# Kernel tuning notes

Measured on AMD Instinct MI355X. Metric: run time of the kernel, lower is better.

## Reference

```python
import jax, jax.numpy as jnp
import numpy as np

N, E, M = 8192, 32768, 2048
D, H1, C = 768, 8, 768
NEG_SLOPE = 0.2


def gat_conv(x, src, dst, W, att_src, att_dst, bias, heads, out_ch):
    # PyG GATConv (eval mode, concat=True, add_self_loops already applied to src/dst)
    n = x.shape[0]
    h = (x @ W).reshape(n, heads, out_ch)                      # [N,H,C]
    a_src = jnp.einsum('nhc,hc->nh', h, att_src)               # [N,H]
    a_dst = jnp.einsum('nhc,hc->nh', h, att_dst)
    e = jax.nn.leaky_relu(a_src[src] + a_dst[dst], NEG_SLOPE)  # [E',H]
    # softmax over incoming edges of each dst node
    m = jax.ops.segment_max(e, dst, num_segments=n)
    e = jnp.exp(e - m[dst])
    denom = jax.ops.segment_sum(e, dst, num_segments=n)
    alpha = e / (denom[dst] + 1e-16)                           # [E',H]
    msg = h[src] * alpha[:, :, None]                           # [E',H,C]
    out = jax.ops.segment_sum(msg, dst, num_segments=n)        # [N,H,C]
    return out.reshape(n, heads * out_ch) + bias


def setup_inputs() -> dict:
    key = jax.random.key(0)
    ks = jax.random.split(key, 16)
    s = 0.02
    inp = {
        'x': jax.random.normal(ks[0], (N, D), jnp.float32),
        'edge_index': jax.random.randint(ks[1], (2, E), 0, N, jnp.int64),
        'mask_idx': jax.random.randint(ks[2], (M,), 0, N, jnp.int64),
        'W1': jax.random.normal(ks[3], (D, H1 * C), jnp.float32) * s,
        'att_src1': jax.random.normal(ks[4], (H1, C), jnp.float32) * s,
        'att_dst1': jax.random.normal(ks[5], (H1, C), jnp.float32) * s,
        'b1': jnp.zeros((H1 * C,), jnp.float32),
        'W2': jax.random.normal(ks[6], (H1 * C, C), jnp.float32) * s,
        'att_src2': jax.random.normal(ks[7], (1, C), jnp.float32) * s,
        'att_dst2': jax.random.normal(ks[8], (1, C), jnp.float32) * s,
        'b2': jnp.zeros((C,), jnp.float32),
        # fc: 1536 -> 768, classifier: 768 -> 2
        'fc_w': jax.random.normal(ks[9], (2 * C, C), jnp.float32) * s,
        'fc_b': jnp.zeros((C,), jnp.float32),
        'cls_w': jax.random.normal(ks[10], (C, 2), jnp.float32) * s,
        'cls_b': jnp.zeros((2,), jnp.float32),
    }
    return inp


def reference(x, edge_index, mask_idx, W1, att_src1, att_dst1, b1,
              W2, att_src2, att_dst2, b2, fc_w, fc_b, cls_w, cls_b):
    n = x.shape[0]
    loops = jnp.arange(n, dtype=edge_index.dtype)
    src = jnp.concatenate([edge_index[0], loops])   # PyG default add_self_loops
    dst = jnp.concatenate([edge_index[1], loops])
    h = gat_conv(x, src, dst, W1, att_src1, att_dst1, b1, H1, C)   # [N, 6144]
    h = jax.nn.elu(h)
    h = gat_conv(h, src, dst, W2, att_src2, att_dst2, b2, 1, C)    # [N, 768]
    x_gemb = h[mask_idx]                                           # [M, 768]
    x_emb = x[mask_idx]                                            # [M, 768]
    out = jnp.concatenate([x_gemb, x_emb], axis=1) @ fc_w + fc_b   # [M, 768]
    out = out @ cls_w + cls_b                                      # [M, 2]
    return out
```

## Files before the change

kernel.cpp:

```cpp
#include <hip/hip_runtime.h>

typedef unsigned short ushort_t;
typedef __attribute__((ext_vector_type(8))) __bf16 bf16x8;
typedef __attribute__((ext_vector_type(8))) unsigned short ushort8;
typedef __attribute__((ext_vector_type(4))) unsigned short ushort4v;
typedef __attribute__((ext_vector_type(4))) float f32x4;

#define N_NODES 8192
#define NODE_MASK 8191
#define E_EDGES 32768
#define E_TOT   40960
#define M_MASK  2048
#define D_IN    768
#define C_CH    768
#define F1      6144

typedef __attribute__((address_space(1))) const void* gas_ptr;
typedef __attribute__((address_space(3))) void* las_ptr;

__device__ __forceinline__ float bf2f(ushort_t u) {
    union { unsigned int i; float f; } v; v.i = ((unsigned int)u) << 16; return v.f;
}
__device__ __forceinline__ ushort_t f2bf(float f) {
    union { float f; unsigned int i; } v; v.f = f;
    unsigned int r = v.i + 0x7fffu + ((v.i >> 16) & 1u);
    return (ushort_t)(r >> 16);
}

__global__ void init_kernel(int* deg, int* fill, int* flags) {
    int i = blockIdx.x * 256 + threadIdx.x;
    if (i < N_NODES) { deg[i] = 0; fill[i] = 0; }
    if (i < 2) flags[i] = 0;
}
__global__ void detect_kernel(const int* __restrict__ raw, int nhalf, int* __restrict__ flag) {
    int i = blockIdx.x * 256 + threadIdx.x;
    if (i < nhalf && raw[2 * i + 1] != 0) atomicOr(flag, 1);
}
__global__ void convert_idx_kernel(const void* __restrict__ raw, int n,
                                   const int* __restrict__ flag, int* __restrict__ out) {
    int i = blockIdx.x * 256 + threadIdx.x;
    if (i >= n) return;
    int v = (*flag) ? ((const int*)raw)[i] : (int)((const long long*)raw)[i];
    out[i] = v & NODE_MASK;
}

__global__ void cvt_bf16_kernel(const float* __restrict__ in, ushort_t* __restrict__ out, int n4) {
    int i = blockIdx.x * 256 + threadIdx.x;
    if (i >= n4) return;
    f32x4 v = *(const f32x4*)(in + i * 4);
    ushort_t o0 = f2bf(v[0]), o1 = f2bf(v[1]), o2 = f2bf(v[2]), o3 = f2bf(v[3]);
    unsigned long long pk = (unsigned long long)o0 | ((unsigned long long)o1 << 16)
                          | ((unsigned long long)o2 << 32) | ((unsigned long long)o3 << 48);
    *(unsigned long long*)(out + i * 4) = pk;
}

__global__ __launch_bounds__(256) void transpose_cvt_kernel(
    const float* __restrict__ in, ushort_t* __restrict__ out, int R, int Ccols)
{
    __shared__ ushort_t tile[32][33];
    int tx = threadIdx.x & 31, ty = threadIdx.x >> 5;
    int x  = blockIdx.x * 32 + tx;
    int y0 = blockIdx.y * 32;
#pragma unroll
    for (int i = 0; i < 4; ++i)
        tile[ty + i * 8][tx] = f2bf(in[(size_t)(y0 + ty + i * 8) * Ccols + x]);
    __syncthreads();
#pragma unroll
    for (int i = 0; i < 4; ++i)
        out[(size_t)(blockIdx.x * 32 + ty + i * 8) * R + y0 + tx] = tile[tx][ty + i * 8];
}

__global__ __launch_bounds__(256) void gemm_bt_kernel(
    const ushort_t* __restrict__ A, const ushort_t* __restrict__ Bt,
    ushort_t* __restrict__ C, const float* __restrict__ bias,
    int M, int N, int K)
{
    __shared__ ushort_t lsA[128 * 64];
    __shared__ ushort_t lsB[128 * 64];

    const int tid  = threadIdx.x;
    const int lane = tid & 63;
    const int wave = tid >> 6;
    const int wm = wave >> 1, wn = wave & 1;
    const int bx = blockIdx.x, by = blockIdx.y;

    const f32x4 zero = {0.f, 0.f, 0.f, 0.f};
    f32x4 acc[4][4];
#pragma unroll
    for (int i = 0; i < 4; ++i)
#pragma unroll
        for (int j = 0; j < 4; ++j) acc[i][j] = zero;

    const int l8 = lane >> 3;
    const int c8 = lane & 7;
    const int q  = lane >> 4;
    const int rl = lane & 15;

    for (int kt = 0; kt < K; kt += 64) {
        __syncthreads();
#pragma unroll
        for (int i = 0; i < 4; ++i) {
            int rbase = wave * 32 + i * 8;
            int row   = rbase + l8;
            int gch   = c8 ^ (row & 7);
            const ushort_t* gA = A  + (size_t)(by * 128 + row) * K + kt + gch * 8;
            const ushort_t* gB = Bt + (size_t)(bx * 128 + row) * K + kt + gch * 8;
            __builtin_amdgcn_global_load_lds((gas_ptr)gA, (las_ptr)(lsA + rbase * 64), 16, 0, 0);
            __builtin_amdgcn_global_load_lds((gas_ptr)gB, (las_ptr)(lsB + rbase * 64), 16, 0, 0);
        }
        __syncthreads();
#pragma unroll
        for (int s = 0; s < 2; ++s) {
            bf16x8 af[4], bfv[4];
#pragma unroll
            for (int i = 0; i < 4; ++i) {
                int Ra = wm * 64 + i * 16 + rl;
                af[i]  = *(const bf16x8*)(lsA + Ra * 64 + (((s * 4 + q) ^ (Ra & 7)) * 8));
                int Rb = wn * 64 + i * 16 + rl;
                bfv[i] = *(const bf16x8*)(lsB + Rb * 64 + (((s * 4 + q) ^ (Rb & 7)) * 8));
            }
#pragma unroll
            for (int i = 0; i < 4; ++i)
#pragma unroll
                for (int j = 0; j < 4; ++j)
                    acc[i][j] = __builtin_amdgcn_mfma_f32_16x16x32_bf16(af[i], bfv[j], acc[i][j], 0, 0, 0);
        }
    }
#pragma unroll
    for (int j = 0; j < 4; ++j) {
        int col = bx * 128 + wn * 64 + j * 16 + rl;
        float bv = bias ? bias[col] : 0.0f;
#pragma unroll
        for (int i = 0; i < 4; ++i) {
#pragma unroll
            for (int t = 0; t < 4; ++t) {
                int row = by * 128 + wm * 64 + i * 16 + q * 4 + t;
                C[(size_t)row * N + col] = f2bf(acc[i][j][t] + bv);
            }
        }
    }
}

#define NBX2 6
#define NBY2 64
#define NSPLIT 2

__global__ __launch_bounds__(256) void gemm_bt_splitk_kernel(
    const ushort_t* __restrict__ A, const ushort_t* __restrict__ Bt,
    float* __restrict__ Cpart, int M, int N, int K)
{
    __shared__ ushort_t lsA[128 * 64];
    __shared__ ushort_t lsB[128 * 64];

    const int tid  = threadIdx.x;
    const int lane = tid & 63;
    const int wave = tid >> 6;
    const int wm = wave >> 1, wn = wave & 1;

    const int d    = blockIdx.x;
    const int xcd  = d & 7;
    const int slot = d >> 3;
    const int bx   = slot % NBX2;
    const int grp  = xcd * 16 + slot / NBX2;
    const int by   = grp & (NBY2 - 1);
    const int bz   = grp >> 6;

    const int kh  = K >> 1;
    const int kt0 = bz * kh;
    float* __restrict__ Cp = Cpart + (size_t)bz * M * N;

    const f32x4 zero = {0.f, 0.f, 0.f, 0.f};
    f32x4 acc[4][4];
#pragma unroll
    for (int i = 0; i < 4; ++i)
#pragma unroll
        for (int j = 0; j < 4; ++j) acc[i][j] = zero;

    const int l8 = lane >> 3;
    const int c8 = lane & 7;
    const int q  = lane >> 4;
    const int rl = lane & 15;

    for (int kt = kt0; kt < kt0 + kh; kt += 64) {
        __syncthreads();
#pragma unroll
        for (int i = 0; i < 4; ++i) {
            int rbase = wave * 32 + i * 8;
            int row   = rbase + l8;
            int gch   = c8 ^ (row & 7);
            const ushort_t* gA = A  + (size_t)(by * 128 + row) * K + kt + gch * 8;
            const ushort_t* gB = Bt + (size_t)(bx * 128 + row) * K + kt + gch * 8;
            __builtin_amdgcn_global_load_lds((gas_ptr)gA, (las_ptr)(lsA + rbase * 64), 16, 0, 0);
            __builtin_amdgcn_global_load_lds((gas_ptr)gB, (las_ptr)(lsB + rbase * 64), 16, 0, 0);
        }
        __syncthreads();
#pragma unroll
        for (int s = 0; s < 2; ++s) {
            bf16x8 af[4], bfv[4];
#pragma unroll
            for (int i = 0; i < 4; ++i) {
                int Ra = wm * 64 + i * 16 + rl;
                af[i]  = *(const bf16x8*)(lsA + Ra * 64 + (((s * 4 + q) ^ (Ra & 7)) * 8));
                int Rb = wn * 64 + i * 16 + rl;
                bfv[i] = *(const bf16x8*)(lsB + Rb * 64 + (((s * 4 + q) ^ (Rb & 7)) * 8));
            }
#pragma unroll
            for (int i = 0; i < 4; ++i)
#pragma unroll
                for (int j = 0; j < 4; ++j)
                    acc[i][j] = __builtin_amdgcn_mfma_f32_16x16x32_bf16(af[i], bfv[j], acc[i][j], 0, 0, 0);
        }
    }
#pragma unroll
    for (int j = 0; j < 4; ++j) {
        int col = bx * 128 + wn * 64 + j * 16 + rl;
#pragma unroll
        for (int i = 0; i < 4; ++i) {
#pragma unroll
            for (int t = 0; t < 4; ++t) {
                int row = by * 128 + wm * 64 + i * 16 + q * 4 + t;
                Cp[(size_t)row * N + col] = acc[i][j][t];
            }
        }
    }
}

__global__ __launch_bounds__(192) void splitk_reduce_att_kernel(
    const float* __restrict__ P0, const float* __restrict__ P1,
    ushort_t* __restrict__ out, const float* __restrict__ as2,
    const float* __restrict__ ad2, float* __restrict__ a_s, float* __restrict__ a_d)
{
    const int n = blockIdx.x, tid = threadIdx.x;
    const int c0 = tid * 4;
    f32x4 a = *(const f32x4*)(P0 + (size_t)n * C_CH + c0);
    f32x4 b = *(const f32x4*)(P1 + (size_t)n * C_CH + c0);
    f32x4 ws = *(const f32x4*)(as2 + c0);
    f32x4 wd = *(const f32x4*)(ad2 + c0);
    float s1 = 0.f, s2 = 0.f;
    ushort_t o[4];
#pragma unroll
    for (int k = 0; k < 4; ++k) {
        float v = a[k] + b[k];
        o[k] = f2bf(v);
        s1 += v * ws[k];
        s2 += v * wd[k];
    }
    unsigned long long pk = (unsigned long long)o[0] | ((unsigned long long)o[1] << 16)
                          | ((unsigned long long)o[2] << 32) | ((unsigned long long)o[3] << 48);
    *(unsigned long long*)(out + (size_t)n * C_CH + c0) = pk;

    __shared__ float red[2][3];
#pragma unroll
    for (int off = 32; off > 0; off >>= 1) {
        s1 += __shfl_down(s1, off);
        s2 += __shfl_down(s2, off);
    }
    const int lane = tid & 63, wv = tid >> 6;
    if (lane == 0) { red[0][wv] = s1; red[1][wv] = s2; }
    __syncthreads();
    if (tid == 0) {
        a_s[n] = red[0][0] + red[0][1] + red[0][2];
        a_d[n] = red[1][0] + red[1][1] + red[1][2];
    }
}

__global__ void indeg_kernel(const int* __restrict__ eic, int* __restrict__ deg) {
    int e = blockIdx.x * 256 + threadIdx.x;
    if (e >= E_TOT) return;
    int dst = (e < E_EDGES) ? eic[E_EDGES + e] : (e - E_EDGES);
    atomicAdd(&deg[dst], 1);
}
__global__ __launch_bounds__(256) void scan_kernel(const int* __restrict__ deg, int* __restrict__ rowptr) {
    __shared__ int part[256];
    int t = threadIdx.x;
    int local[32];
    int s = 0;
#pragma unroll
    for (int i = 0; i < 32; ++i) { local[i] = deg[t * 32 + i]; s += local[i]; }
    part[t] = s;
    __syncthreads();
    for (int off = 1; off < 256; off <<= 1) {
        int v = (t >= off) ? part[t - off] : 0;
        __syncthreads();
        part[t] += v;
        __syncthreads();
    }
    int run = (t == 0) ? 0 : part[t - 1];
#pragma unroll
    for (int i = 0; i < 32; ++i) { rowptr[t * 32 + i] = run; run += local[i]; }
    if (t == 255) rowptr[N_NODES] = run;
}
__global__ void scatter_kernel(const int* __restrict__ eic, const int* __restrict__ rowptr,
                               int* __restrict__ fill, int* __restrict__ csr_src) {
    int e = blockIdx.x * 256 + threadIdx.x;
    if (e >= E_TOT) return;
    int src, dst;
    if (e < E_EDGES) { src = eic[e]; dst = eic[E_EDGES + e]; }
    else             { src = e - E_EDGES; dst = src; }
    int pos = rowptr[dst] + atomicAdd(&fill[dst], 1);
    csr_src[pos] = src;
}

__global__ __launch_bounds__(256) void att_kernel(
    const ushort_t* __restrict__ h, const float* __restrict__ att_s,
    const float* __restrict__ att_d, float* __restrict__ a_s, float* __restrict__ a_d,
    int heads, int stride)
{
    int gid  = blockIdx.x * 4 + (threadIdx.x >> 6);
    int lane = threadIdx.x & 63;
    int n = gid / heads, hd = gid % heads;
    const ushort_t* hp = h + (size_t)n * stride + hd * C_CH;
    const float* sp = att_s + hd * C_CH;
    const float* dp = att_d + hd * C_CH;
    float s1 = 0.f, s2 = 0.f;
#pragma unroll
    for (int j = 0; j < 3; ++j) {
        int o = j * 256 + lane * 4;
        ushort4v hv = *(const ushort4v*)(hp + o);
        f32x4 sv = *(const f32x4*)(sp + o);
        f32x4 dv = *(const f32x4*)(dp + o);
#pragma unroll
        for (int k = 0; k < 4; ++k) {
            float f = bf2f(hv[k]);
            s1 += f * sv[k];
            s2 += f * dv[k];
        }
    }
#pragma unroll
    for (int off = 32; off > 0; off >>= 1) {
        s1 += __shfl_down(s1, off);
        s2 += __shfl_down(s2, off);
    }
    if (lane == 0) { a_s[gid] = s1; a_d[gid] = s2; }
}

__global__ __launch_bounds__(192) void agg8_kernel(
    const ushort_t* __restrict__ h, const float* __restrict__ a_s, const float* __restrict__ a_d,
    const int* __restrict__ rowptr, const int* __restrict__ csr_src,
    const float* __restrict__ bias, ushort_t* __restrict__ out)
{
    const int n = blockIdx.x;
    const int half = blockIdx.y;
    const int tid = threadIdx.x;
    const int base = rowptr[n];
    const int deg  = rowptr[n + 1] - base;

    __shared__ float s_m[8], s_rd[8], s_adst[8];
    __shared__ int   s_src[64];
    __shared__ float s_w[64][8];

    if (tid < 8) {
        float adst = a_d[n * 8 + tid];
        float m = -1e30f;
        for (int e = 0; e < deg; ++e) {
            float scv = a_s[csr_src[base + e] * 8 + tid] + adst;
            scv = scv > 0.f ? scv : 0.2f * scv;
            m = fmaxf(m, scv);
        }
        float den = 0.f;
        for (int e = 0; e < deg; ++e) {
            float scv = a_s[csr_src[base + e] * 8 + tid] + adst;
            scv = scv > 0.f ? scv : 0.2f * scv;
            den += __expf(scv - m);
        }
        s_m[tid] = m; s_rd[tid] = 1.0f / (den + 1e-16f); s_adst[tid] = adst;
    }
    __syncthreads();

    float acc[16];
#pragma unroll
    for (int i = 0; i < 16; ++i) acc[i] = 0.f;
    const int c0   = half * 3072 + tid * 16;
    const int myhd = (half << 2) + tid / 48;

    for (int cs = 0; cs < deg; cs += 64) {
        int cnt = min(64, deg - cs);
        __syncthreads();
        for (int idx = tid; idx < cnt; idx += 192) s_src[idx] = csr_src[base + cs + idx];
        __syncthreads();
        for (int idx = tid; idx < cnt * 8; idx += 192) {
            int e = idx >> 3, hd = idx & 7;
            float scv = a_s[s_src[e] * 8 + hd] + s_adst[hd];
            scv = scv > 0.f ? scv : 0.2f * scv;
            s_w[e][hd] = __expf(scv - s_m[hd]) * s_rd[hd];
        }
        __syncthreads();
        int e = 0;
        for (; e + 1 < cnt; e += 2) {
            const ushort_t* hp0 = h + (size_t)s_src[e] * F1 + c0;
            const ushort_t* hp1 = h + (size_t)s_src[e + 1] * F1 + c0;
            ushort8 a0 = *(const ushort8*)(hp0);
            ushort8 a1 = *(const ushort8*)(hp0 + 8);
            ushort8 b0 = *(const ushort8*)(hp1);
            ushort8 b1 = *(const ushort8*)(hp1 + 8);
            float w0 = s_w[e][myhd], w1 = s_w[e + 1][myhd];
#pragma unroll
            for (int i = 0; i < 8; ++i) {
                acc[i]     += w0 * bf2f(a0[i]) + w1 * bf2f(b0[i]);
                acc[8 + i] += w0 * bf2f(a1[i]) + w1 * bf2f(b1[i]);
            }
        }
        if (e < cnt) {
            const ushort_t* hp0 = h + (size_t)s_src[e] * F1 + c0;
            ushort8 a0 = *(const ushort8*)(hp0);
            ushort8 a1 = *(const ushort8*)(hp0 + 8);
            float w0 = s_w[e][myhd];
#pragma unroll
            for (int i = 0; i < 8; ++i) {
                acc[i]     += w0 * bf2f(a0[i]);
                acc[8 + i] += w0 * bf2f(a1[i]);
            }
        }
    }
#pragma unroll
    for (int i = 0; i < 16; ++i) {
        float v = acc[i] + bias[c0 + i];
        v = v > 0.f ? v : (__expf(v) - 1.0f);
        out[(size_t)n * F1 + c0 + i] = f2bf(v);
    }
}

__global__ __launch_bounds__(256) void agg1_kernel(
    const ushort_t* __restrict__ h, const float* __restrict__ a_s, const float* __restrict__ a_d,
    const int* __restrict__ rowptr, const int* __restrict__ csr_src,
    const float* __restrict__ bias, ushort_t* __restrict__ out)
{
    const int n = blockIdx.x;
    const int tid = threadIdx.x;
    const int base = rowptr[n];
    const int deg  = rowptr[n + 1] - base;
    __shared__ float s_m, s_rd, s_adst;
    __shared__ int   s_src[64];
    __shared__ float s_w[64];
    if (tid == 0) {
        float adst = a_d[n];
        float m = -1e30f;
        for (int e = 0; e < deg; ++e) {
            float scv = a_s[csr_src[base + e]] + adst;
            scv = scv > 0.f ? scv : 0.2f * scv;
            m = fmaxf(m, scv);
        }
        float den = 0.f;
        for (int e = 0; e < deg; ++e) {
            float scv = a_s[csr_src[base + e]] + adst;
            scv = scv > 0.f ? scv : 0.2f * scv;
            den += __expf(scv - m);
        }
        s_m = m; s_rd = 1.0f / (den + 1e-16f); s_adst = adst;
    }
    __syncthreads();
    float acc0 = 0.f, acc1 = 0.f, acc2 = 0.f;
    const int c0 = tid * 3;
    for (int cs = 0; cs < deg; cs += 64) {
        int cnt = min(64, deg - cs);
        __syncthreads();
        for (int idx = tid; idx < cnt; idx += 256) s_src[idx] = csr_src[base + cs + idx];
        __syncthreads();
        for (int idx = tid; idx < cnt; idx += 256) {
            float scv = a_s[s_src[idx]] + s_adst;
            scv = scv > 0.f ? scv : 0.2f * scv;
            s_w[idx] = __expf(scv - s_m) * s_rd;
        }
        __syncthreads();
        for (int e = 0; e < cnt; ++e) {
            const ushort_t* hp = h + (size_t)s_src[e] * C_CH + c0;
            float w = s_w[e];
            acc0 += w * bf2f(hp[0]);
            acc1 += w * bf2f(hp[1]);
            acc2 += w * bf2f(hp[2]);
        }
    }
    out[(size_t)n * C_CH + c0 + 0] = f2bf(acc0 + bias[c0 + 0]);
    out[(size_t)n * C_CH + c0 + 1] = f2bf(acc1 + bias[c0 + 1]);
    out[(size_t)n * C_CH + c0 + 2] = f2bf(acc2 + bias[c0 + 2]);
}

__global__ void gatherfc_kernel(const ushort_t* __restrict__ out2, const ushort_t* __restrict__ xb,
                                const int* __restrict__ maskc, ushort_t* __restrict__ Afc)
{
    int m = blockIdx.x, t = threadIdx.x;
    int mi = maskc[m];
    const ushort_t* p1 = out2 + (size_t)mi * 768;
    const ushort_t* p2 = xb   + (size_t)mi * 768;
    for (int c = t; c < 768; c += 256) {
        Afc[(size_t)m * 1536 + c]       = p1[c];
        Afc[(size_t)m * 1536 + 768 + c] = p2[c];
    }
}

__global__ __launch_bounds__(256) void cls_kernel(
    const ushort_t* __restrict__ fc_out, const float* __restrict__ cls_w,
    const float* __restrict__ cls_b, float* __restrict__ out)
{
    int m = blockIdx.x * 4 + (threadIdx.x >> 6);
    int lane = threadIdx.x & 63;
    float a0 = 0.f, a1 = 0.f;
    const ushort_t* row = fc_out + (size_t)m * 768;
    for (int i = lane; i < 768; i += 64) {
        float v = bf2f(row[i]);
        a0 += v * cls_w[i * 2 + 0];
        a1 += v * cls_w[i * 2 + 1];
    }
#pragma unroll
    for (int off = 32; off > 0; off >>= 1) {
        a0 += __shfl_down(a0, off);
        a1 += __shfl_down(a1, off);
    }
    if (lane == 0) {
        out[m * 2 + 0] = a0 + cls_b[0];
        out[m * 2 + 1] = a1 + cls_b[1];
    }
}

extern "C" void kernel_launch(void* const* d_in, const int* in_sizes, int n_in,
                              void* d_out, int out_size, void* d_ws, size_t ws_size,
                              hipStream_t stream)
{
    const float* x        = (const float*)d_in[0];
    const void*  ei_raw   = d_in[1];
    const void*  mask_raw = d_in[2];
    const float* W1       = (const float*)d_in[3];
    const float* att_src1 = (const float*)d_in[4];
    const float* att_dst1 = (const float*)d_in[5];
    const float* b1       = (const float*)d_in[6];
    const float* W2       = (const float*)d_in[7];
    const float* att_src2 = (const float*)d_in[8];
    const float* att_dst2 = (const float*)d_in[9];
    const float* b2       = (const float*)d_in[10];
    const float* fc_w     = (const float*)d_in[11];
    const float* fc_b     = (const float*)d_in[12];
    const float* cls_w    = (const float*)d_in[13];
    const float* cls_b    = (const float*)d_in[14];
    float* out = (float*)d_out;

    char* ws = (char*)d_ws;
    size_t off = 0;
    auto alloc = [&](size_t bytes) { char* p = ws + off; off = (off + bytes + 255) & ~(size_t)255; return p; };
    int*   flags  = (int*)alloc(2 * 4);
    int*   eic    = (int*)alloc((size_t)2 * E_EDGES * 4);
    int*   maskc  = (int*)alloc((size_t)M_MASK * 4);
    int*   deg    = (int*)alloc(N_NODES * 4);
    int*   fill   = (int*)alloc(N_NODES * 4);
    int*   rowptr = (int*)alloc((N_NODES + 1) * 4);
    int*   csr    = (int*)alloc(E_TOT * 4);
    float* a_s1   = (float*)alloc((size_t)N_NODES * 8 * 4);
    float* a_d1   = (float*)alloc((size_t)N_NODES * 8 * 4);
    float* a_s2   = (float*)alloc((size_t)N_NODES * 4);
    float* a_d2   = (float*)alloc((size_t)N_NODES * 4);
    ushort_t* W1t  = (ushort_t*)alloc((size_t)D_IN * F1 * 2);
    ushort_t* W2t  = (ushort_t*)alloc((size_t)F1 * C_CH * 2);
    ushort_t* fcwt = (ushort_t*)alloc((size_t)1536 * 768 * 2);
    ushort_t* xb   = (ushort_t*)alloc((size_t)N_NODES * D_IN * 2);
    char* region1 = alloc((size_t)N_NODES * F1 * 2);
    char* region2 = alloc((size_t)N_NODES * F1 * 2);
    ushort_t* h1    = (ushort_t*)region1;
    ushort_t* h2    = (ushort_t*)region1;
    ushort_t* Afc   = (ushort_t*)(region1 + (16u << 20));
    ushort_t* fcout = (ushort_t*)(region1 + (32u << 20));
    float*    part  = (float*)(region1 + (48u << 20));
    ushort_t* out1  = (ushort_t*)region2;
    ushort_t* out2  = (ushort_t*)region2;

    init_kernel<<<N_NODES / 256, 256, 0, stream>>>(deg, fill, flags);
    detect_kernel<<<(E_EDGES + 255) / 256, 256, 0, stream>>>((const int*)ei_raw, E_EDGES, &flags[0]);
    detect_kernel<<<(M_MASK / 2 + 255) / 256, 256, 0, stream>>>((const int*)mask_raw, M_MASK / 2, &flags[1]);
    convert_idx_kernel<<<(2 * E_EDGES + 255) / 256, 256, 0, stream>>>(ei_raw, 2 * E_EDGES, &flags[0], eic);
    convert_idx_kernel<<<(M_MASK + 255) / 256, 256, 0, stream>>>(mask_raw, M_MASK, &flags[1], maskc);
    indeg_kernel<<<E_TOT / 256, 256, 0, stream>>>(eic, deg);
    scan_kernel<<<1, 256, 0, stream>>>(deg, rowptr);
    scatter_kernel<<<E_TOT / 256, 256, 0, stream>>>(eic, rowptr, fill, csr);

    cvt_bf16_kernel<<<(N_NODES * D_IN / 4 + 255) / 256, 256, 0, stream>>>(x, xb, N_NODES * D_IN / 4);
    transpose_cvt_kernel<<<dim3(F1 / 32, D_IN / 32), 256, 0, stream>>>(W1, W1t, D_IN, F1);
    transpose_cvt_kernel<<<dim3(C_CH / 32, F1 / 32), 256, 0, stream>>>(W2, W2t, F1, C_CH);
    transpose_cvt_kernel<<<dim3(768 / 32, 1536 / 32), 256, 0, stream>>>(fc_w, fcwt, 1536, 768);

    gemm_bt_kernel<<<dim3(F1 / 128, N_NODES / 128), 256, 0, stream>>>(xb, W1t, h1, nullptr, N_NODES, F1, D_IN);
    att_kernel<<<(N_NODES * 8) / 4, 256, 0, stream>>>(h1, att_src1, att_dst1, a_s1, a_d1, 8, F1);
    agg8_kernel<<<dim3(N_NODES, 2), 192, 0, stream>>>(h1, a_s1, a_d1, rowptr, csr, b1, out1);

    gemm_bt_splitk_kernel<<<NBX2 * NBY2 * NSPLIT, 256, 0, stream>>>(out1, W2t, part, N_NODES, C_CH, F1);
    splitk_reduce_att_kernel<<<N_NODES, 192, 0, stream>>>(
        part, part + (size_t)N_NODES * C_CH, h2, att_src2, att_dst2, a_s2, a_d2);
    agg1_kernel<<<N_NODES, 256, 0, stream>>>(h2, a_s2, a_d2, rowptr, csr, b2, out2);

    gatherfc_kernel<<<M_MASK, 256, 0, stream>>>(out2, xb, maskc, Afc);
    gemm_bt_kernel<<<dim3(768 / 128, M_MASK / 128), 256, 0, stream>>>(Afc, fcwt, fcout, fc_b, M_MASK, 768, 1536);
    cls_kernel<<<M_MASK / 4, 256, 0, stream>>>(fcout, cls_w, cls_b, out);
}
```

Before: 520.0 us.

## Precompute W1·att vectors for layer-1 attention and warp-per-node agg1

Layer-1 attention logits are now computed as x·(W1·att) by folding the attention vectors into W1 up front, followed by a small GEMV over x. This replaces the pass that read the whole 8192×6144 bf16 h1 tensor. Separately, agg1 is rewritten to give each 64-lane wavefront one node, with a parallel max and sum over edges and vectorised 12-channel loads broadcast via shuffles, replacing a single-thread softmax and several block barriers. The algebraic reordering changes rounding slightly, since fp32 x·W1 is used instead of the bf16 h1.

```diff
diff --git a/kernel.cpp b/kernel.cpp
--- a/kernel.cpp
+++ b/kernel.cpp
@@ -301,37 +301,69 @@
     csr_src[pos] = src;
 }
 
-__global__ __launch_bounds__(256) void att_kernel(
-    const ushort_t* __restrict__ h, const float* __restrict__ att_s,
-    const float* __restrict__ att_d, float* __restrict__ a_s, float* __restrict__ a_d,
-    int heads, int stride)
+__global__ __launch_bounds__(256) void att1_wprep_kernel(
+    const float* __restrict__ W1, const float* __restrict__ att_s,
+    const float* __restrict__ att_d, float* __restrict__ ws, float* __restrict__ wd)
 {
     int gid  = blockIdx.x * 4 + (threadIdx.x >> 6);
     int lane = threadIdx.x & 63;
-    int n = gid / heads, hd = gid % heads;
-    const ushort_t* hp = h + (size_t)n * stride + hd * C_CH;
-    const float* sp = att_s + hd * C_CH;
-    const float* dp = att_d + hd * C_CH;
+    int d = gid >> 3, h = gid & 7;
+    const float* wp = W1 + (size_t)d * F1 + h * C_CH;
+    const float* sp = att_s + h * C_CH;
+    const float* dp = att_d + h * C_CH;
     float s1 = 0.f, s2 = 0.f;
 #pragma unroll
     for (int j = 0; j < 3; ++j) {
         int o = j * 256 + lane * 4;
-        ushort4v hv = *(const ushort4v*)(hp + o);
+        f32x4 w  = *(const f32x4*)(wp + o);
         f32x4 sv = *(const f32x4*)(sp + o);
         f32x4 dv = *(const f32x4*)(dp + o);
 #pragma unroll
-        for (int k = 0; k < 4; ++k) {
-            float f = bf2f(hv[k]);
-            s1 += f * sv[k];
-            s2 += f * dv[k];
-        }
+        for (int k = 0; k < 4; ++k) { s1 += w[k] * sv[k]; s2 += w[k] * dv[k]; }
     }
 #pragma unroll
     for (int off = 32; off > 0; off >>= 1) {
         s1 += __shfl_down(s1, off);
         s2 += __shfl_down(s2, off);
     }
-    if (lane == 0) { a_s[gid] = s1; a_d[gid] = s2; }
+    if (lane == 0) { ws[d * 8 + h] = s1; wd[d * 8 + h] = s2; }
+}
+
+__global__ __launch_bounds__(256) void att1_gemv_kernel(
+    const ushort_t* __restrict__ xb, const float* __restrict__ ws,
+    const float* __restrict__ wd, float* __restrict__ a_s, float* __restrict__ a_d)
+{
+    int n    = blockIdx.x * 4 + (threadIdx.x >> 6);
+    int lane = threadIdx.x & 63;
+    const ushort_t* xp = xb + (size_t)n * D_IN;
+    float s[8], d[8];
+#pragma unroll
+    for (int h = 0; h < 8; ++h) { s[h] = 0.f; d[h] = 0.f; }
+#pragma unroll
+    for (int j = 0; j < 3; ++j) {
+        int d0 = j * 256 + lane * 4;
+        ushort4v xv = *(const ushort4v*)(xp + d0);
+#pragma unroll
+        for (int k = 0; k < 4; ++k) {
+            float xf = bf2f(xv[k]);
+            const float* wr = ws + (size_t)(d0 + k) * 8;
+            const float* dr = wd + (size_t)(d0 + k) * 8;
+#pragma unroll
+            for (int h = 0; h < 8; ++h) { s[h] += xf * wr[h]; d[h] += xf * dr[h]; }
+        }
+    }
+#pragma unroll
+    for (int h = 0; h < 8; ++h) {
+#pragma unroll
+        for (int off = 32; off > 0; off >>= 1) {
+            s[h] += __shfl_down(s[h], off);
+            d[h] += __shfl_down(d[h], off);
+        }
+    }
+    if (lane == 0) {
+#pragma unroll
+        for (int h = 0; h < 8; ++h) { a_s[n * 8 + h] = s[h]; a_d[n * 8 + h] = d[h]; }
+    }
 }
 
 __global__ __launch_bounds__(192) void agg8_kernel(
@@ -425,54 +457,76 @@
     const int* __restrict__ rowptr, const int* __restrict__ csr_src,
     const float* __restrict__ bias, ushort_t* __restrict__ out)
 {
-    const int n = blockIdx.x;
-    const int tid = threadIdx.x;
+    const int n    = blockIdx.x * 4 + (threadIdx.x >> 6);
+    const int lane = threadIdx.x & 63;
     const int base = rowptr[n];
     const int deg  = rowptr[n + 1] - base;
-    __shared__ float s_m, s_rd, s_adst;
-    __shared__ int   s_src[64];
-    __shared__ float s_w[64];
-    if (tid == 0) {
-        float adst = a_d[n];
-        float m = -1e30f;
-        for (int e = 0; e < deg; ++e) {
+    const float adst = a_d[n];
+
+    float m = -1e30f;
+    for (int cs = 0; cs < deg; cs += 64) {
+        int e = cs + lane;
+        if (e < deg) {
             float scv = a_s[csr_src[base + e]] + adst;
             scv = scv > 0.f ? scv : 0.2f * scv;
             m = fmaxf(m, scv);
         }
-        float den = 0.f;
-        for (int e = 0; e < deg; ++e) {
+    }
+#pragma unroll
+    for (int off = 32; off > 0; off >>= 1) m = fmaxf(m, __shfl_xor(m, off));
+    float den = 0.f;
+    for (int cs = 0; cs < deg; cs += 64) {
+        int e = cs + lane;
+        if (e < deg) {
             float scv = a_s[csr_src[base + e]] + adst;
             scv = scv > 0.f ? scv : 0.2f * scv;
             den += __expf(scv - m);
         }
-        s_m = m; s_rd = 1.0f / (den + 1e-16f); s_adst = adst;
-    }
-    __syncthreads();
-    float acc0 = 0.f, acc1 = 0.f, acc2 = 0.f;
-    const int c0 = tid * 3;
+    }
+#pragma unroll
+    for (int off = 32; off > 0; off >>= 1) den += __shfl_xor(den, off);
+    const float rd = 1.0f / (den + 1e-16f);
+
+    const int c0 = lane * 12;
+    float acc[12];
+#pragma unroll
+    for (int i = 0; i < 12; ++i) acc[i] = 0.f;
+
     for (int cs = 0; cs < deg; cs += 64) {
         int cnt = min(64, deg - cs);
-        __syncthreads();
-        for (int idx = tid; idx < cnt; idx += 256) s_src[idx] = csr_src[base + cs + idx];
-        __syncthreads();
-        for (int idx = tid; idx < cnt; idx += 256) {
-            float scv = a_s[s_src[idx]] + s_adst;
+        int e = cs + lane;
+        int srcl = (e < deg) ? csr_src[base + e] : 0;
+        float wv = 0.f;
+        if (e < deg) {
+            float scv = a_s[srcl] + adst;
             scv = scv > 0.f ? scv : 0.2f * scv;
-            s_w[idx] = __expf(scv - s_m) * s_rd;
-        }
-        __syncthreads();
-        for (int e = 0; e < cnt; ++e) {
-            const ushort_t* hp = h + (size_t)s_src[e] * C_CH + c0;
-            float w = s_w[e];
-            acc0 += w * bf2f(hp[0]);
-            acc1 += w * bf2f(hp[1]);
-            acc2 += w * bf2f(hp[2]);
-        }
-    }
-    out[(size_t)n * C_CH + c0 + 0] = f2bf(acc0 + bias[c0 + 0]);
-    out[(size_t)n * C_CH + c0 + 1] = f2bf(acc1 + bias[c0 + 1]);
-    out[(size_t)n * C_CH + c0 + 2] = f2bf(acc2 + bias[c0 + 2]);
+            wv = __expf(scv - m) * rd;
+        }
+        for (int k = 0; k < cnt; ++k) {
+            int src = __shfl(srcl, k);
+            float w = __shfl(wv, k);
+            const ushort_t* hp = h + (size_t)src * C_CH + c0;
+            ushort4v v0 = *(const ushort4v*)(hp);
+            ushort4v v1 = *(const ushort4v*)(hp + 4);
+            ushort4v v2 = *(const ushort4v*)(hp + 8);
+#pragma unroll
+            for (int i = 0; i < 4; ++i) {
+                acc[i]     += w * bf2f(v0[i]);
+                acc[4 + i] += w * bf2f(v1[i]);
+                acc[8 + i] += w * bf2f(v2[i]);
+            }
+        }
+    }
+#pragma unroll
+    for (int p = 0; p < 3; ++p) {
+        ushort_t o0 = f2bf(acc[p * 4 + 0] + bias[c0 + p * 4 + 0]);
+        ushort_t o1 = f2bf(acc[p * 4 + 1] + bias[c0 + p * 4 + 1]);
+        ushort_t o2 = f2bf(acc[p * 4 + 2] + bias[c0 + p * 4 + 2]);
+        ushort_t o3 = f2bf(acc[p * 4 + 3] + bias[c0 + p * 4 + 3]);
+        unsigned long long pk = (unsigned long long)o0 | ((unsigned long long)o1 << 16)
+                              | ((unsigned long long)o2 << 32) | ((unsigned long long)o3 << 48);
+        *(unsigned long long*)(out + (size_t)n * C_CH + c0 + p * 4) = pk;
+    }
 }
 
 __global__ void gatherfc_kernel(const ushort_t* __restrict__ out2, const ushort_t* __restrict__ xb,
@@ -547,6 +601,8 @@
     float* a_d1   = (float*)alloc((size_t)N_NODES * 8 * 4);
     float* a_s2   = (float*)alloc((size_t)N_NODES * 4);
     float* a_d2   = (float*)alloc((size_t)N_NODES * 4);
+    float* ws1    = (float*)alloc((size_t)D_IN * 8 * 4);
+    float* wd1    = (float*)alloc((size_t)D_IN * 8 * 4);
     ushort_t* W1t  = (ushort_t*)alloc((size_t)D_IN * F1 * 2);
     ushort_t* W2t  = (ushort_t*)alloc((size_t)F1 * C_CH * 2);
     ushort_t* fcwt = (ushort_t*)alloc((size_t)1536 * 768 * 2);
@@ -574,15 +630,16 @@
     transpose_cvt_kernel<<<dim3(F1 / 32, D_IN / 32), 256, 0, stream>>>(W1, W1t, D_IN, F1);
     transpose_cvt_kernel<<<dim3(C_CH / 32, F1 / 32), 256, 0, stream>>>(W2, W2t, F1, C_CH);
     transpose_cvt_kernel<<<dim3(768 / 32, 1536 / 32), 256, 0, stream>>>(fc_w, fcwt, 1536, 768);
+    att1_wprep_kernel<<<(D_IN * 8) / 4, 256, 0, stream>>>(W1, att_src1, att_dst1, ws1, wd1);
 
     gemm_bt_kernel<<<dim3(F1 / 128, N_NODES / 128), 256, 0, stream>>>(xb, W1t, h1, nullptr, N_NODES, F1, D_IN);
-    att_kernel<<<(N_NODES * 8) / 4, 256, 0, stream>>>(h1, att_src1, att_dst1, a_s1, a_d1, 8, F1);
+    att1_gemv_kernel<<<N_NODES / 4, 256, 0, stream>>>(xb, ws1, wd1, a_s1, a_d1);
     agg8_kernel<<<dim3(N_NODES, 2), 192, 0, stream>>>(h1, a_s1, a_d1, rowptr, csr, b1, out1);
 
     gemm_bt_splitk_kernel<<<NBX2 * NBY2 * NSPLIT, 256, 0, stream>>>(out1, W2t, part, N_NODES, C_CH, F1);
     splitk_reduce_att_kernel<<<N_NODES, 192, 0, stream>>>(
         part, part + (size_t)N_NODES * C_CH, h2, att_src2, att_dst2, a_s2, a_d2);
-    agg1_kernel<<<N_NODES, 256, 0, stream>>>(h2, a_s2, a_d2, rowptr, csr, b2, out2);
+    agg1_kernel<<<N_NODES / 4, 256, 0, stream>>>(h2, a_s2, a_d2, rowptr, csr, b2, out2);
 
     gatherfc_kernel<<<M_MASK, 256, 0, stream>>>(out2, xb, maskc, Afc);
     gemm_bt_kernel<<<dim3(768 / 128, M_MASK / 128), 256, 0, stream>>>(Afc, fcwt, fcout, fc_b, M_MASK, 768, 1536);
```

Result: slower. 538.0 us (+3.5%).
